# Kernel optimization log

Measured on AMD Instinct MI355X. Metric: run time of the kernel, lower is better.

Reference implementation:

```python
import jax, jax.numpy as jnp
import numpy as np

NUM_HEADS = 12


def setup_inputs() -> dict:
    key = jax.random.key(0)
    k1, k2, k3, k4 = jax.random.split(key, 4)
    B, N, C = 8, 1024, 768
    x = jax.random.normal(k1, (B, N, C), dtype=jnp.float32)
    # nn.Linear(dim, 3*dim, bias=False): weight applied as x @ W, shape [C, 3C]
    w_qkv = jax.random.normal(k2, (C, 3 * C), dtype=jnp.float32) * (C ** -0.5)
    # nn.Linear(dim, dim) with bias
    w_proj = jax.random.normal(k3, (C, C), dtype=jnp.float32) * (C ** -0.5)
    b_proj = jax.random.normal(k4, (C,), dtype=jnp.float32) * 0.01
    return {"x": x, "w_qkv": w_qkv, "w_proj": w_proj, "b_proj": b_proj, "H": 32, "W": 32}


def reference(x, w_qkv, w_proj, b_proj, H, W):
    B, N, C = x.shape
    nh = NUM_HEADS
    hd = C // nh
    scale = hd ** -0.5
    qkv = (x @ w_qkv).reshape(B, N, 3, nh, hd)
    q, k, v = jnp.moveaxis(qkv, 2, 0)  # each [B, N, nh, hd]
    attn = jnp.einsum("bnhd,bmhd->bhnm", q, k) * scale  # [B, nh, N, N]
    attn = jax.nn.softmax(attn, axis=-1)
    out = jnp.einsum("bhnm,bmhd->bnhd", attn, v).reshape(B, N, C)
    return out @ w_proj + b_proj
```

## Files before the change

kernel.cpp:

```cpp
#include <hip/hip_runtime.h>

typedef __bf16 bf16x8 __attribute__((ext_vector_type(8)));
typedef float f32x4 __attribute__((ext_vector_type(4)));
typedef unsigned short u16;
typedef unsigned int u32;
typedef u16 u16x4 __attribute__((ext_vector_type(4)));

__device__ __forceinline__ u16 f2bf(float f) {
    union { float f; u32 u; } x{f};
    u32 r = x.u + 0x7FFFu + ((x.u >> 16) & 1u);
    return (u16)(r >> 16);
}

__device__ __forceinline__ float ex2(float x) {
#if __has_builtin(__builtin_amdgcn_exp2f)
    return __builtin_amdgcn_exp2f(x);
#else
    return __expf(x * 0.6931471805599453f);
#endif
}

#define GLD16(g, l)                                                            \
    __builtin_amdgcn_global_load_lds(                                          \
        (const __attribute__((address_space(1))) u32*)(g),                     \
        (__attribute__((address_space(3))) u32*)(l), 16, 0, 0)

__global__ void convert_bf16(const float* __restrict__ src, u16* __restrict__ dst, int n4) {
    int i = blockIdx.x * blockDim.x + threadIdx.x;
    if (i < n4) {
        float4 f = *(const float4*)(src + (size_t)i * 4);
        u16x4 u = { f2bf(f.x), f2bf(f.y), f2bf(f.z), f2bf(f.w) };
        *(u16x4*)(dst + (size_t)i * 4) = u;
    }
}

__global__ __launch_bounds__(256) void prep_weights(
    const float* __restrict__ wq, const float* __restrict__ wp,
    u16* __restrict__ WqT, u16* __restrict__ WpT)
{
    __shared__ u16 tile[32][33];
    int id = blockIdx.x;
    const float* src; u16* dst; int R, C, bx, by;
    if (id < 1728) { src = wq; dst = WqT; R = 768; C = 2304; bx = (id % 72) * 32; by = (id / 72) * 32; }
    else { id -= 1728; src = wp; dst = WpT; R = 768; C = 768; bx = (id % 24) * 32; by = (id / 24) * 32; }
    int x = threadIdx.x & 31, y = threadIdx.x >> 5;
    #pragma unroll
    for (int i = 0; i < 32; i += 8)
        tile[y + i][x] = f2bf(src[(size_t)(by + y + i) * C + bx + x]);
    __syncthreads();
    #pragma unroll
    for (int i = 0; i < 32; i += 8)
        dst[(size_t)(bx + y + i) * R + by + x] = tile[x][y + i];
}

template <int K>
__global__ __launch_bounds__(256) void gemm_qkv(
    const u16* __restrict__ A,
    const u16* __restrict__ Wt,
    u16* __restrict__ QKV,
    u16* __restrict__ Vt,
    float qscale)
{
    __shared__ __align__(16) u16 As[128 * 64];
    __shared__ __align__(16) u16 Bs[128 * 64];

    int tid = threadIdx.x;
    int wave = tid >> 6, lane = tid & 63;
    int quad = lane >> 4, l16 = lane & 15;
    int wm = (wave >> 1) * 64, wn = (wave & 1) * 64;
    int bm = blockIdx.y * 128, bn = blockIdx.x * 128;
    bool vsec = (bn >= 1536);

    f32x4 acc[4][4] = {};

    int srow = lane >> 3;
    int scg = ((lane & 7) ^ srow) * 8;
    const u16* Ap = A + (size_t)(bm + wave * 32 + srow) * K + scg;
    const u16* Bp = Wt + (size_t)(bn + wave * 32 + srow) * K + scg;

    int fg0 = (((0 * 4 + quad) ^ (l16 & 7)) * 8);
    int fg1 = (((1 * 4 + quad) ^ (l16 & 7)) * 8);

    for (int k0 = 0; k0 < K; k0 += 64) {
        #pragma unroll
        for (int j = 0; j < 4; j++) {
            GLD16(Ap + k0 + (size_t)j * 8 * K, &As[(wave * 32 + j * 8) * 64]);
            GLD16(Bp + k0 + (size_t)j * 8 * K, &Bs[(wave * 32 + j * 8) * 64]);
        }
        __syncthreads();

        #pragma unroll
        for (int h = 0; h < 2; h++) {
            int fg = h ? fg1 : fg0;
            bf16x8 af[4], bfr[4];
            #pragma unroll
            for (int i = 0; i < 4; i++) {
                af[i]  = *(const bf16x8*)&As[(wm + i * 16 + l16) * 64 + fg];
                bfr[i] = *(const bf16x8*)&Bs[(wn + i * 16 + l16) * 64 + fg];
            }
            if (!vsec) {
                #pragma unroll
                for (int mi = 0; mi < 4; mi++)
                    #pragma unroll
                    for (int ni = 0; ni < 4; ni++)
                        acc[mi][ni] = __builtin_amdgcn_mfma_f32_16x16x32_bf16(af[mi], bfr[ni], acc[mi][ni], 0, 0, 0);
            } else {
                #pragma unroll
                for (int mi = 0; mi < 4; mi++)
                    #pragma unroll
                    for (int ni = 0; ni < 4; ni++)
                        acc[mi][ni] = __builtin_amdgcn_mfma_f32_16x16x32_bf16(bfr[ni], af[mi], acc[mi][ni], 0, 0, 0);
            }
        }
        __syncthreads();
    }

    if (!vsec) {
        #pragma unroll
        for (int mi = 0; mi < 4; mi++) {
            #pragma unroll
            for (int ni = 0; ni < 4; ni++) {
                #pragma unroll
                for (int rg = 0; rg < 4; rg++) {
                    int row = bm + wm + mi * 16 + quad * 4 + rg;
                    int col = bn + wn + ni * 16 + l16;
                    float sc = (col < 768) ? qscale : 1.0f;
                    QKV[(size_t)row * 2304 + col] = f2bf(acc[mi][ni][rg] * sc);
                }
            }
        }
    } else {
        #pragma unroll
        for (int mi = 0; mi < 4; mi++) {
            #pragma unroll
            for (int ni = 0; ni < 4; ni++) {
                #pragma unroll
                for (int rg = 0; rg < 4; rg++) {
                    int d = (bn - 1536) + wn + ni * 16 + quad * 4 + rg;
                    int ng = bm + wm + mi * 16 + l16;
                    int b = ng >> 10, n = ng & 1023, h = d >> 6;
                    Vt[((size_t)(b * 12 + h) * 64 + (d & 63)) * 1024 + n] = f2bf(acc[mi][ni][rg]);
                }
            }
        }
    }
}

template <int K>
__global__ __launch_bounds__(256) void gemm_proj(
    const u16* __restrict__ A,
    const u16* __restrict__ Bt,
    float* __restrict__ Cp,
    const float* __restrict__ bias,
    int M, int N)
{
    __shared__ __align__(16) u16 As[128 * 64];
    __shared__ __align__(16) u16 Bs[128 * 64];

    int tid = threadIdx.x;
    int wave = tid >> 6, lane = tid & 63;
    int quad = lane >> 4, l16 = lane & 15;
    int wm = (wave >> 1) * 64, wn = (wave & 1) * 64;
    int bm = blockIdx.y * 128, bn = blockIdx.x * 128;

    f32x4 acc[4][4] = {};

    int srow = lane >> 3;
    int scg = ((lane & 7) ^ srow) * 8;
    const u16* Ap = A + (size_t)(bm + wave * 32 + srow) * K + scg;
    const u16* Bp = Bt + (size_t)(bn + wave * 32 + srow) * K + scg;

    int fg0 = (((0 * 4 + quad) ^ (l16 & 7)) * 8);
    int fg1 = (((1 * 4 + quad) ^ (l16 & 7)) * 8);

    for (int k0 = 0; k0 < K; k0 += 64) {
        #pragma unroll
        for (int j = 0; j < 4; j++) {
            GLD16(Ap + k0 + (size_t)j * 8 * K, &As[(wave * 32 + j * 8) * 64]);
            GLD16(Bp + k0 + (size_t)j * 8 * K, &Bs[(wave * 32 + j * 8) * 64]);
        }
        __syncthreads();

        #pragma unroll
        for (int h = 0; h < 2; h++) {
            int fg = h ? fg1 : fg0;
            bf16x8 af[4], bfr[4];
            #pragma unroll
            for (int i = 0; i < 4; i++) {
                af[i]  = *(const bf16x8*)&As[(wm + i * 16 + l16) * 64 + fg];
                bfr[i] = *(const bf16x8*)&Bs[(wn + i * 16 + l16) * 64 + fg];
            }
            #pragma unroll
            for (int mi = 0; mi < 4; mi++)
                #pragma unroll
                for (int ni = 0; ni < 4; ni++)
                    acc[mi][ni] = __builtin_amdgcn_mfma_f32_16x16x32_bf16(af[mi], bfr[ni], acc[mi][ni], 0, 0, 0);
        }
        __syncthreads();
    }

    #pragma unroll
    for (int mi = 0; mi < 4; mi++) {
        #pragma unroll
        for (int ni = 0; ni < 4; ni++) {
            #pragma unroll
            for (int rg = 0; rg < 4; rg++) {
                int row = bm + wm + mi * 16 + quad * 4 + rg;
                int col = bn + wn + ni * 16 + l16;
                Cp[(size_t)row * N + col] = acc[mi][ni][rg] + bias[col];
            }
        }
    }
}

__global__ __launch_bounds__(256, 4) void attn_kernel(
    const u16* __restrict__ qkv,
    const u16* __restrict__ Vt,
    u16* __restrict__ ctx)
{
    __shared__ __align__(16) u16 Ks[2][4096];
    __shared__ __align__(16) u16 Vs[2][4096];
    __shared__ __align__(16) u16 Ps[4096];

    int qt = blockIdx.x;
    int bh = blockIdx.y;
    int b = bh / 12, h = bh % 12;
    int tid = threadIdx.x;
    int wave = tid >> 6, lane = tid & 63;
    int quad = lane >> 4, l16 = lane & 15;

    int sw8 = (quad ^ (l16 & 7)) * 8;

    int qrow = qt * 64 + wave * 16 + l16;
    const u16* qbase = qkv + (size_t)(b * 1024 + qrow) * 2304 + h * 64;
    bf16x8 qf0 = *(const bf16x8*)(qbase + quad * 8);
    bf16x8 qf1 = *(const bf16x8*)(qbase + 32 + quad * 8);

    int srow = lane >> 3;
    int scol = (lane & 7) ^ srow;
    const u16* kA = qkv + (size_t)(b * 1024 + wave * 16 + srow) * 2304 + 768 + h * 64 + scol * 8;
    const u16* vA = Vt + ((size_t)bh * 64 + wave * 16 + srow) * 1024 + scol * 8;

    bf16x8 ones;
    #pragma unroll
    for (int j = 0; j < 8; j++) ((u16*)&ones)[j] = 0x3F80;

    f32x4 o[4] = {};
    f32x4 lsum = {};

    {
        GLD16(kA,            &Ks[0][(wave * 2 + 0) * 512]);
        GLD16(kA + 8 * 2304, &Ks[0][(wave * 2 + 1) * 512]);
        GLD16(vA,            &Vs[0][(wave * 2 + 0) * 512]);
        GLD16(vA + 8 * 1024, &Vs[0][(wave * 2 + 1) * 512]);
    }

    #pragma unroll 2
    for (int kt = 0; kt < 16; kt++) {
        int buf = kt & 1;
        __syncthreads();

        if (kt < 15) {
            const u16* k0 = kA + (size_t)(kt + 1) * (64 * 2304);
            const u16* v0 = vA + (size_t)(kt + 1) * 64;
            GLD16(k0,            &Ks[buf ^ 1][(wave * 2 + 0) * 512]);
            GLD16(k0 + 8 * 2304, &Ks[buf ^ 1][(wave * 2 + 1) * 512]);
            GLD16(v0,            &Vs[buf ^ 1][(wave * 2 + 0) * 512]);
            GLD16(v0 + 8 * 1024, &Vs[buf ^ 1][(wave * 2 + 1) * 512]);
        }

        f32x4 s[4];
        #pragma unroll
        for (int nb = 0; nb < 4; nb++) {
            int rbase = (nb * 16 + l16) * 64;
            bf16x8 kf0 = *(const bf16x8*)&Ks[buf][rbase + sw8];
            bf16x8 kf1 = *(const bf16x8*)&Ks[buf][rbase + (sw8 ^ 32)];
            f32x4 z = {};
            z = __builtin_amdgcn_mfma_f32_16x16x32_bf16(qf0, kf0, z, 0, 0, 0);
            z = __builtin_amdgcn_mfma_f32_16x16x32_bf16(qf1, kf1, z, 0, 0, 0);
            s[nb] = z;
        }

        #pragma unroll
        for (int nb = 0; nb < 4; nb++) {
            #pragma unroll
            for (int rg = 0; rg < 4; rg++) {
                float p = ex2(s[nb][rg]);
                union { float f; u32 u; } c{p};
                u16 pb = (u16)((c.u + 0x8000u) >> 16);
                int row = quad * 4 + rg;
                int cgr = (nb * 2 + (l16 >> 3)) ^ (row & 7);
                Ps[wave * 1024 + row * 64 + cgr * 8 + (l16 & 7)] = pb;
            }
        }
        asm volatile("s_waitcnt lgkmcnt(0)" ::: "memory");

        bf16x8 pf0 = *(const bf16x8*)&Ps[wave * 1024 + l16 * 64 + sw8];
        bf16x8 pf1 = *(const bf16x8*)&Ps[wave * 1024 + l16 * 64 + (sw8 ^ 32)];

        lsum = __builtin_amdgcn_mfma_f32_16x16x32_bf16(pf0, ones, lsum, 0, 0, 0);
        lsum = __builtin_amdgcn_mfma_f32_16x16x32_bf16(pf1, ones, lsum, 0, 0, 0);

        #pragma unroll
        for (int db = 0; db < 4; db++) {
            int rbase = (db * 16 + l16) * 64;
            bf16x8 vf0 = *(const bf16x8*)&Vs[buf][rbase + sw8];
            bf16x8 vf1 = *(const bf16x8*)&Vs[buf][rbase + (sw8 ^ 32)];
            o[db] = __builtin_amdgcn_mfma_f32_16x16x32_bf16(pf0, vf0, o[db], 0, 0, 0);
            o[db] = __builtin_amdgcn_mfma_f32_16x16x32_bf16(pf1, vf1, o[db], 0, 0, 0);
        }
    }

    float rl[4];
    #pragma unroll
    for (int rg = 0; rg < 4; rg++) rl[rg] = 1.0f / lsum[rg];
    #pragma unroll
    for (int db = 0; db < 4; db++) {
        #pragma unroll
        for (int rg = 0; rg < 4; rg++) {
            int row = qt * 64 + wave * 16 + quad * 4 + rg;
            int col = h * 64 + db * 16 + l16;
            ctx[(size_t)(b * 1024 + row) * 768 + col] = f2bf(o[db][rg] * rl[rg]);
        }
    }
}

extern "C" void kernel_launch(void* const* d_in, const int* in_sizes, int n_in,
                              void* d_out, int out_size, void* d_ws, size_t ws_size,
                              hipStream_t stream) {
    const float* x      = (const float*)d_in[0];
    const float* w_qkv  = (const float*)d_in[1];
    const float* w_proj = (const float*)d_in[2];
    const float* b_proj = (const float*)d_in[3];
    float* out = (float*)d_out;

    const int BN = 8192;
    const int C = 768, C3 = 2304;
    const float CE = 0.18033688011112042f;

    u16* Xb      = (u16*)d_ws;
    u16* Wqkv_t  = Xb + (size_t)BN * C;
    u16* Wproj_t = Wqkv_t + (size_t)C3 * C;
    u16* QKV     = Wproj_t + (size_t)C * C;
    u16* Vt      = QKV + (size_t)BN * C3;
    u16* Ctx     = Vt + (size_t)96 * 64 * 1024;

    convert_bf16<<<(BN * C / 4 + 255) / 256, 256, 0, stream>>>(x, Xb, BN * C / 4);
    prep_weights<<<2304, 256, 0, stream>>>(w_qkv, w_proj, Wqkv_t, Wproj_t);

    gemm_qkv<768><<<dim3(C3 / 128, BN / 128), 256, 0, stream>>>(
        Xb, Wqkv_t, QKV, Vt, CE);

    attn_kernel<<<dim3(16, 96), 256, 0, stream>>>(QKV, Vt, Ctx);

    gemm_proj<768><<<dim3(C / 128, BN / 128), 256, 0, stream>>>(
        Ctx, Wproj_t, out, b_proj, BN, C);
}
```

Before: 199.6 us.

## Use 32x32x16 MFMA with 128-row query tiles in attention kernel

Attention switches from 16x16x32 to 32x32x16 bf16 MFMA. Each wave now handles 32 query rows, so a block covers 128 queries and the grid halves. Each K/V tile loaded into LDS is reused across twice as many queries, and the wider MFMA cuts instruction count per FLOP. In exchange it uses more accumulator registers, a larger P buffer in LDS, lower occupancy bounds (3 blocks per CU) and only 768 blocks.

```diff
diff --git a/kernel.cpp b/kernel.cpp
--- a/kernel.cpp
+++ b/kernel.cpp
@@ -2,6 +2,7 @@
 
 typedef __bf16 bf16x8 __attribute__((ext_vector_type(8)));
 typedef float f32x4 __attribute__((ext_vector_type(4)));
+typedef float f32x16 __attribute__((ext_vector_type(16)));
 typedef unsigned short u16;
 typedef unsigned int u32;
 typedef u16 u16x4 __attribute__((ext_vector_type(4)));
@@ -213,28 +214,28 @@
     }
 }
 
-__global__ __launch_bounds__(256, 4) void attn_kernel(
+__global__ __launch_bounds__(256, 3) void attn_kernel(
     const u16* __restrict__ qkv,
     const u16* __restrict__ Vt,
     u16* __restrict__ ctx)
 {
     __shared__ __align__(16) u16 Ks[2][4096];
     __shared__ __align__(16) u16 Vs[2][4096];
-    __shared__ __align__(16) u16 Ps[4096];
+    __shared__ __align__(16) u16 Ps[8192];
 
     int qt = blockIdx.x;
     int bh = blockIdx.y;
     int b = bh / 12, h = bh % 12;
     int tid = threadIdx.x;
     int wave = tid >> 6, lane = tid & 63;
-    int quad = lane >> 4, l16 = lane & 15;
-
-    int sw8 = (quad ^ (l16 & 7)) * 8;
-
-    int qrow = qt * 64 + wave * 16 + l16;
-    const u16* qbase = qkv + (size_t)(b * 1024 + qrow) * 2304 + h * 64;
-    bf16x8 qf0 = *(const bf16x8*)(qbase + quad * 8);
-    bf16x8 qf1 = *(const bf16x8*)(qbase + 32 + quad * 8);
+    int l32 = lane & 31, half = lane >> 5;
+    int l7 = lane & 7;
+
+    const u16* qbase = qkv + (size_t)(b * 1024 + qt * 128 + wave * 32 + l32) * 2304 + h * 64;
+    bf16x8 qa[4];
+    #pragma unroll
+    for (int ks = 0; ks < 4; ks++)
+        qa[ks] = *(const bf16x8*)(qbase + ks * 16 + half * 8);
 
     int srow = lane >> 3;
     int scol = (lane & 7) ^ srow;
@@ -245,8 +246,12 @@
     #pragma unroll
     for (int j = 0; j < 8; j++) ((u16*)&ones)[j] = 0x3F80;
 
-    f32x4 o[4] = {};
-    f32x4 lsum = {};
+    f32x16 o0 = {}, o1 = {}, lsum = {};
+
+    int fgo[4];
+    #pragma unroll
+    for (int ks = 0; ks < 4; ks++)
+        fgo[ks] = (((ks * 2 + half) ^ l7) * 8);
 
     {
         GLD16(kA,            &Ks[0][(wave * 2 + 0) * 512]);
@@ -269,59 +274,50 @@
             GLD16(v0 + 8 * 1024, &Vs[buf ^ 1][(wave * 2 + 1) * 512]);
         }
 
-        f32x4 s[4];
-        #pragma unroll
-        for (int nb = 0; nb < 4; nb++) {
-            int rbase = (nb * 16 + l16) * 64;
-            bf16x8 kf0 = *(const bf16x8*)&Ks[buf][rbase + sw8];
-            bf16x8 kf1 = *(const bf16x8*)&Ks[buf][rbase + (sw8 ^ 32)];
-            f32x4 z = {};
-            z = __builtin_amdgcn_mfma_f32_16x16x32_bf16(qf0, kf0, z, 0, 0, 0);
-            z = __builtin_amdgcn_mfma_f32_16x16x32_bf16(qf1, kf1, z, 0, 0, 0);
-            s[nb] = z;
-        }
-
-        #pragma unroll
-        for (int nb = 0; nb < 4; nb++) {
-            #pragma unroll
-            for (int rg = 0; rg < 4; rg++) {
-                float p = ex2(s[nb][rg]);
+        f32x16 s0 = {}, s1 = {};
+        #pragma unroll
+        for (int ks = 0; ks < 4; ks++) {
+            bf16x8 k0 = *(const bf16x8*)&Ks[buf][(l32)      * 64 + fgo[ks]];
+            bf16x8 k1 = *(const bf16x8*)&Ks[buf][(32 + l32) * 64 + fgo[ks]];
+            s0 = __builtin_amdgcn_mfma_f32_32x32x16_bf16(qa[ks], k0, s0, 0, 0, 0);
+            s1 = __builtin_amdgcn_mfma_f32_32x32x16_bf16(qa[ks], k1, s1, 0, 0, 0);
+        }
+
+        int k3a = l32 >> 3;
+        #pragma unroll
+        for (int nb = 0; nb < 2; nb++) {
+            int kg = nb * 4 + k3a;
+            #pragma unroll
+            for (int reg = 0; reg < 16; reg++) {
+                float sv = nb ? s1[reg] : s0[reg];
+                float p = ex2(sv);
                 union { float f; u32 u; } c{p};
                 u16 pb = (u16)((c.u + 0x8000u) >> 16);
-                int row = quad * 4 + rg;
-                int cgr = (nb * 2 + (l16 >> 3)) ^ (row & 7);
-                Ps[wave * 1024 + row * 64 + cgr * 8 + (l16 & 7)] = pb;
+                int row = (reg & 3) + 8 * (reg >> 2) + 4 * half;
+                Ps[wave * 2048 + row * 64 + ((kg ^ (row & 7)) * 8) + l7] = pb;
             }
         }
         asm volatile("s_waitcnt lgkmcnt(0)" ::: "memory");
 
-        bf16x8 pf0 = *(const bf16x8*)&Ps[wave * 1024 + l16 * 64 + sw8];
-        bf16x8 pf1 = *(const bf16x8*)&Ps[wave * 1024 + l16 * 64 + (sw8 ^ 32)];
-
-        lsum = __builtin_amdgcn_mfma_f32_16x16x32_bf16(pf0, ones, lsum, 0, 0, 0);
-        lsum = __builtin_amdgcn_mfma_f32_16x16x32_bf16(pf1, ones, lsum, 0, 0, 0);
-
-        #pragma unroll
-        for (int db = 0; db < 4; db++) {
-            int rbase = (db * 16 + l16) * 64;
-            bf16x8 vf0 = *(const bf16x8*)&Vs[buf][rbase + sw8];
-            bf16x8 vf1 = *(const bf16x8*)&Vs[buf][rbase + (sw8 ^ 32)];
-            o[db] = __builtin_amdgcn_mfma_f32_16x16x32_bf16(pf0, vf0, o[db], 0, 0, 0);
-            o[db] = __builtin_amdgcn_mfma_f32_16x16x32_bf16(pf1, vf1, o[db], 0, 0, 0);
-        }
-    }
-
-    float rl[4];
-    #pragma unroll
-    for (int rg = 0; rg < 4; rg++) rl[rg] = 1.0f / lsum[rg];
-    #pragma unroll
-    for (int db = 0; db < 4; db++) {
-        #pragma unroll
-        for (int rg = 0; rg < 4; rg++) {
-            int row = qt * 64 + wave * 16 + quad * 4 + rg;
-            int col = h * 64 + db * 16 + l16;
-            ctx[(size_t)(b * 1024 + row) * 768 + col] = f2bf(o[db][rg] * rl[rg]);
-        }
+        #pragma unroll
+        for (int ks = 0; ks < 4; ks++) {
+            bf16x8 pf = *(const bf16x8*)&Ps[wave * 2048 + l32 * 64 + fgo[ks]];
+            bf16x8 v0 = *(const bf16x8*)&Vs[buf][(l32)      * 64 + fgo[ks]];
+            bf16x8 v1 = *(const bf16x8*)&Vs[buf][(32 + l32) * 64 + fgo[ks]];
+            lsum = __builtin_amdgcn_mfma_f32_32x32x16_bf16(pf, ones, lsum, 0, 0, 0);
+            o0   = __builtin_amdgcn_mfma_f32_32x32x16_bf16(pf, v0, o0, 0, 0, 0);
+            o1   = __builtin_amdgcn_mfma_f32_32x32x16_bf16(pf, v1, o1, 0, 0, 0);
+        }
+    }
+
+    #pragma unroll
+    for (int reg = 0; reg < 16; reg++) {
+        float inv = 1.0f / lsum[reg];
+        int row = (reg & 3) + 8 * (reg >> 2) + 4 * half;
+        int qrow = qt * 128 + wave * 32 + row;
+        size_t base = (size_t)(b * 1024 + qrow) * 768 + h * 64 + l32;
+        ctx[base]      = f2bf(o0[reg] * inv);
+        ctx[base + 32] = f2bf(o1[reg] * inv);
     }
 }
 
@@ -351,7 +347,7 @@
     gemm_qkv<768><<<dim3(C3 / 128, BN / 128), 256, 0, stream>>>(
         Xb, Wqkv_t, QKV, Vt, CE);
 
-    attn_kernel<<<dim3(16, 96), 256, 0, stream>>>(QKV, Vt, Ctx);
+    attn_kernel<<<dim3(8, 96), 256, 0, stream>>>(QKV, Vt, Ctx);
 
     gemm_proj<768><<<dim3(C / 128, BN / 128), 256, 0, stream>>>(
         Ctx, Wproj_t, out, b_proj, BN, C);
```

Result: no change. 197.2 us (-1.2%).
